# Kernel tuning notes

Measured on AMD Instinct MI355X. Metric: run time of the kernel, lower is better.

The kernel has to match this reference:

```python
import jax, jax.numpy as jnp
import numpy as np

M = 32          # option['m']
ETA = 1e-4      # option['eta']
THRES = 1e-12
NUM_DATA = 20000
NUM_FEAT = 1024


def setup_inputs() -> dict:
    key = jax.random.key(0)
    k1, k2 = jax.random.split(key)
    inputs_matrix = jax.random.normal(k1, (NUM_DATA, NUM_FEAT), dtype=jnp.float32)
    outputs = jax.random.normal(k2, (NUM_DATA,), dtype=jnp.float32)
    return {"inputs_matrix": inputs_matrix, "outputs": outputs}


def reference(inputs_matrix, outputs):
    """SFTRL_CCFM.online_learning (task='reg').

    Note on faithfulness: in the original torch code the negative-sketch
    branch (sign > 0) is guarded by `elif self.row_count_n == 2*m - 1`, and
    row_count_n starts at 0 and is only incremented inside that branch, so
    it is unreachable; BT_N stays identically zero and contributes 0 to
    `scalar`. We therefore only carry the positive sketch BT_P.
    """
    m, eta, thres = M, ETA, THRES
    two_m = 2 * m
    d = inputs_matrix.shape[1]

    def shrink(BT_P):
        # Frequent-Directions style shrink via SVD of the 2m x 2m Gram matrix.
        G = BT_P.T @ BT_P                                  # (2m, 2m)
        U, S, _ = jnp.linalg.svd(G)                        # S sorted descending
        S = jnp.where(S <= thres, 0.0, S)
        nnz = jnp.sum(S > 0).astype(jnp.int32)
        inv_sqrt = jnp.where(S > 0, 1.0 / jnp.sqrt(jnp.where(S > 0, S, 1.0)), 0.0)
        V = (BT_P @ U) * inv_sqrt[None, :]                 # (d, 2m); cols >= nnz are 0
        j = jnp.arange(two_m)
        # nnz >= m branch: keep m-1 cols scaled by sqrt(S_j - S_m), zero-pad rest.
        scale_big = jnp.where(j < m - 1, jnp.sqrt(jnp.maximum(S - S[m], 0.0)), 0.0)
        # nnz < m branch: keep nnz cols scaled by sqrt(S_j), zero-pad rest.
        scale_small = jnp.where(j < nnz, jnp.sqrt(S), 0.0)
        ge = nnz >= m
        scale = jnp.where(ge, scale_big, scale_small)
        return V * scale[None, :], jnp.where(ge, jnp.int32(m - 1), nnz)

    def step(carry, xs):
        BT_P, rc_p = carry
        alpha, bi = xs                                     # alpha: (d,)
        BPa = BT_P.T @ alpha                               # (2m,)
        scalar = BPa @ BPa                                 # BT_N == 0 -> its term vanishes
        sign = 2.0 * (scalar - bi)                         # grad of squared loss (task='reg')

        def do_update(args):
            B, rc = args
            rc = rc + 1                                    # original writes AFTER incrementing
            B = B.at[:, rc].set(jnp.sqrt(-eta * sign) * alpha)
            B, rc = jax.lax.cond(rc == two_m - 1, shrink, lambda Bp: (Bp, rc), B)
            return B, rc

        BT_P, rc_p = jax.lax.cond(sign <= 0.0, do_update, lambda a: a, (BT_P, rc_p))
        return (BT_P, rc_p), scalar

    init = (jnp.zeros((d, two_m), inputs_matrix.dtype), jnp.int32(0))
    _, preds = jax.lax.scan(step, init, (inputs_matrix, outputs))
    return preds
```

## Files before the change

### kernel.cpp

```cpp
#include <hip/hip_runtime.h>
#include <hip/hip_cooperative_groups.h>
#include <math.h>

namespace cg = cooperative_groups;

#define NDATA   20000
#define DFEAT   1024
#define TWO_M   64
#define MM      32
#define ETA_F   1e-4f
#define THRES_F 1e-12f
#define NSWEEP  8
#define NBLK    256
#define NTHR    1024
#define NW      (NBLK*(NTHR/64))
#define CH      384
#define BIGF    3.0e38f

#define O_CTL    0
#define O_CNT    256
#define O_ACCT   1280
#define O_ACCK   1536
#define O_TTIME  1792
#define O_BT     2048
#define O_BASE   264192
#define O_SCV    344192
#define O_FLAG   424192
#define O_CL0    504192
#define O_LA     584192
#define O_LB     664192
#define O_CHT    744192
#define O_CHB    746240
#define O_CHS    748288
#define O_D      750336

#define C_NACC 0
#define C_RC   1
#define C_SHR  2
#define C_TS   3
#define C_RCA  4
#define C_DONE 5

#define TG(r,c)     SH[(r)*257 + (c)]
#define SG(cb,idx)  SH[16448 + (cb)*4096 + (idx)]
#define SU(cb,idx)  SH[24640 + (cb)*4096 + (idx)]

__device__ __forceinline__ float wave_sum(float v) {
    v += __shfl_xor(v, 1);  v += __shfl_xor(v, 2);  v += __shfl_xor(v, 4);
    v += __shfl_xor(v, 8);  v += __shfl_xor(v, 16); v += __shfl_xor(v, 32);
    return v;
}
__device__ __forceinline__ int wave_min_i(int v) {
    v = min(v, __shfl_xor(v, 1));  v = min(v, __shfl_xor(v, 2));
    v = min(v, __shfl_xor(v, 4));  v = min(v, __shfl_xor(v, 8));
    v = min(v, __shfl_xor(v, 16)); v = min(v, __shfl_xor(v, 32));
    return v;
}
__device__ __forceinline__ void pair_from(int p, int &a, int &b) {
    int a_ = 0, rem = p;
    while (rem >= 64 - a_) { rem -= 64 - a_; ++a_; }
    a = a_; b = a_ + rem;
}
__device__ __forceinline__ float dot16(float4 x0, float4 x1, float4 x2, float4 x3,
                                       float4 y0, float4 y1, float4 y2, float4 y3) {
    float d = x0.x*y0.x + x0.y*y0.y + x0.z*y0.z + x0.w*y0.w;
    d += x1.x*y1.x + x1.y*y1.y + x1.z*y1.z + x1.w*y1.w;
    d += x2.x*y2.x + x2.y*y2.y + x2.z*y2.z + x2.w*y2.w;
    d += x3.x*y3.x + x3.y*y3.y + x3.z*y3.z + x3.w*y3.w;
    return d;
}
__device__ __forceinline__ int lbound(const int* arr, int n, int key) {
    int lo = 0, hi = n;
    while (lo < hi) { int mid = (lo + hi) >> 1; if (arr[mid] > key) hi = mid; else lo = mid + 1; }
    return lo;
}

__device__ void finalize_range(const float* __restrict__ A, const float* __restrict__ base,
                               const float* __restrict__ Bt, const int* __restrict__ ttime,
                               float* __restrict__ out,
                               int lo, int hi, int jlo, int jhi, int gw, int lane)
{
    for (int t = lo + gw; t <= hi; t += NW) {
        const float4* At = (const float4*)(A + (size_t)t * DFEAT);
        float4 a0 = At[lane*4+0], a1 = At[lane*4+1], a2 = At[lane*4+2], a3 = At[lane*4+3];
        float o = base[t];
        for (int jc = jlo; jc <= jhi; ++jc) {
            if (ttime[jc] >= t) break;
            const float4* Bj = (const float4*)(Bt + (size_t)jc * DFEAT);
            float d = dot16(a0, a1, a2, a3,
                            Bj[lane*4+0], Bj[lane*4+1], Bj[lane*4+2], Bj[lane*4+3]);
            d = wave_sum(d);
            o += d * d;
        }
        if (lane == 0) out[t] = o;
    }
}

__device__ void build_D(const float* __restrict__ A, const int* __restrict__ listP,
                        int clen, float* __restrict__ D, int w, int lane)
{
    if (w >= CH * 8) return;
    int i  = w >> 3;
    int of = w & 7;
    if (i >= clen) return;
    const float4* Ai = (const float4*)(A + (size_t)listP[i] * DFEAT);
    float4 a0 = Ai[lane*4+0], a1 = Ai[lane*4+1], a2 = Ai[lane*4+2], a3 = Ai[lane*4+3];
    for (int j = i + 1 + of; j < clen; j += 8) {
        const float4* Aj = (const float4*)(A + (size_t)listP[j] * DFEAT);
        float d = dot16(a0, a1, a2, a3,
                        Aj[lane*4+0], Aj[lane*4+1], Aj[lane*4+2], Aj[lane*4+3]);
        d = wave_sum(d);
        if (lane == 0) D[(size_t)i * CH + j] = d;
    }
}

__device__ void phase_prepare(const float* __restrict__ A, const float* __restrict__ Y,
                              float* __restrict__ scv, int* __restrict__ flag,
                              const int* __restrict__ listP, int lenL,
                              const int* __restrict__ accT, const float* __restrict__ accK, int nacc,
                              int* __restrict__ chT, float* __restrict__ chB, float* __restrict__ chS,
                              float* __restrict__ D, int* __restrict__ counts,
                              float* SH, int* s_cnt,
                              int bid, int tid, int wv, int lane, int gw)
{
    int clen = min(lenL, CH);
    for (int i = bid * NTHR + tid; i < clen; i += NBLK * NTHR) {
        int t = listP[i];
        chT[i] = t;
        chB[i] = Y[t];
    }
    const int hs = (CH + NBLK - 1) / NBLK;
    int h0 = min(bid * hs, clen), h1 = min(h0 + hs, clen);
    int tailLen = lenL > CH ? lenL - CH : 0;
    int ts2 = (tailLen + NBLK - 1) / NBLK;
    int t0 = CH + min(bid * ts2, tailLen), t1 = min(t0 + ts2, lenL);
    if (tid == 0) *s_cnt = 0;
    __syncthreads();

    for (int jb = 0; jb < nacc; jb += 16) {
        int nj = min(16, nacc - jb);
        if (wv < nj) {
            const float4* Ar = (const float4*)(A + (size_t)accT[jb + wv] * DFEAT);
            float4* S4 = (float4*)SH;
            for (int q = 0; q < 4; ++q) S4[wv * 256 + lane * 4 + q] = Ar[lane * 4 + q];
        }
        __syncthreads();
        const float4* S4 = (const float4*)SH;
        for (int pass = 0; pass < 2; ++pass) {
            int lo = pass ? t0 : h0, hi = pass ? t1 : h1;
            for (int e = lo + wv; e < hi; e += 16) {
                int t = listP[e];
                const float4* At = (const float4*)(A + (size_t)t * DFEAT);
                float4 a0 = At[lane*4+0], a1 = At[lane*4+1], a2 = At[lane*4+2], a3 = At[lane*4+3];
                float cacc = 0.f;
                for (int j = 0; j < nj; ++j) {
                    float d = dot16(a0, a1, a2, a3,
                                    S4[j*256+lane*4+0], S4[j*256+lane*4+1],
                                    S4[j*256+lane*4+2], S4[j*256+lane*4+3]);
                    d = wave_sum(d);
                    float v = accK[jb + j] * d;
                    cacc += v * v;
                }
                if (lane == 0) scv[t] += cacc;
            }
        }
        __syncthreads();
    }

    for (int e = h0 + tid; e < h1; e += NTHR) {
        int t = listP[e];
        float sc = scv[t];
        int alive = (sc <= Y[t]) ? 1 : 0;
        flag[t] = alive;
        chS[e] = alive ? sc : BIGF;
    }
    for (int e = t0 + tid; e < t1; e += NTHR) {
        int t = listP[e];
        float sc = scv[t];
        int alive = (sc <= Y[t]) ? 1 : 0;
        flag[t] = alive;
        if (alive) atomicAdd(s_cnt, 1);
    }
    __syncthreads();
    if (tid == 0) counts[bid] = *s_cnt;

    build_D(A, listP, clen, D, gw, lane);
}

__device__ int scatter_and_total(const int* __restrict__ listCur, int lenCur,
                                 const int* __restrict__ flag, const int* __restrict__ counts,
                                 int* __restrict__ listNxt, int bid, int tid, int wv, int lane)
{
    int tailLen = lenCur > CH ? lenCur - CH : 0;
    int ts2 = (tailLen + NBLK - 1) / NBLK;
    int e0 = min(bid * ts2, tailLen), e1 = min(e0 + ts2, tailLen);
    if (wv == 0 && e1 > e0) {
        int dst = 0;
        for (int b = 0; b < bid; ++b) dst += counts[b];
        for (int w0 = e0; w0 < e1; w0 += 64) {
            int idx = w0 + lane;
            int tt = 0, fl = 0;
            if (idx < e1) { tt = listCur[CH + idx]; fl = flag[tt]; }
            unsigned long long mb = __ballot(fl);
            int pos = (int)__popcll(mb & ((1ull << lane) - 1ull));
            if (fl) listNxt[dst + pos] = tt;
            dst += (int)__popcll(mb);
        }
    }
    int tot = 0;
    for (int b = 0; b < NBLK; ++b) tot += counts[b];
    return tot;
}

__device__ void resolve_blk0(const float* __restrict__ A, float* __restrict__ Bt,
                             int* __restrict__ ttime,
                             const int* __restrict__ chT, const float* __restrict__ chB,
                             const float* __restrict__ chS, const float* __restrict__ D,
                             int* __restrict__ ctl, int* __restrict__ accT, float* __restrict__ accK,
                             int chunkLen, int tailTotal,
                             float* accL, float* bbL, int* s_red, int* s_imin,
                             int* accTl, float* accKl, int tid, int wv, int lane)
{
    int rc0 = ctl[C_RC];
    if (tid < CH) {
        accL[tid] = (tid < chunkLen) ? chS[tid] : BIGF;
        bbL[tid]  = (tid < chunkLen) ? chB[tid] : -BIGF;
    }
    __syncthreads();
    int rcl = rc0, naccL = 0, shr = 0, tsv = NDATA;
    for (;;) {
        int cand = 0x7FFFFFFF;
        if (tid < chunkLen && accL[tid] <= bbL[tid]) cand = tid;
        cand = wave_min_i(cand);
        if (lane == 0) s_red[wv] = cand;
        __syncthreads();
        if (wv == 0) {
            int v = (lane < 16) ? s_red[lane] : 0x7FFFFFFF;
            v = wave_min_i(v);
            if (lane == 0) *s_imin = v;
        }
        __syncthreads();
        int im = *s_imin;
        if (im == 0x7FFFFFFF) break;
        float sc = accL[im], b = bbL[im];
        float kap = sqrtf(2.f * ETA_F * (b - sc));
        __syncthreads();
        rcl += 1;
        if (tid == 0) { accTl[naccL] = chT[im]; accKl[naccL] = kap; }
        naccL += 1;
        if (tid > im && tid < chunkLen) {
            float dv = D[(size_t)im * CH + tid];
            float v = kap * dv;
            accL[tid] += v * v;
        }
        if (tid <= im && tid < CH) accL[tid] = BIGF;
        if (rcl == TWO_M - 1) { shr = 1; tsv = chT[im]; }
        __syncthreads();
        if (shr) break;
    }
    __syncthreads();
    for (int q = 0; q < naccL; ++q) {
        int colr = rc0 + 1 + q;
        int tq = accTl[q];
        float kq = accKl[q];
        Bt[(size_t)colr * DFEAT + tid] = kq * A[(size_t)tq * DFEAT + tid];
        if (tid == 0) ttime[colr] = tq;
    }
    if (tid < naccL) { accT[tid] = accTl[tid]; accK[tid] = accKl[tid]; }
    if (tid == 0) {
        ctl[C_NACC] = naccL;
        ctl[C_RC]   = rcl;
        ctl[C_SHR]  = shr;
        ctl[C_TS]   = tsv;
        ctl[C_DONE] = (!shr && naccL == 0 && tailTotal == 0) ? 1 : 0;
    }
}

__device__ void jacobi_shrink(float* __restrict__ Bt, int* __restrict__ ctl, float* SH,
                              float* s_rotA, float* s_rotB, int* s_prt,
                              float* s_S, float* s_Ss, int* s_perm, int* s_misc, int tid)
{
    float acc0 = 0.f, acc1 = 0.f, acc2 = 0.f;
    int a0i, b0i, a1i, b1i, a2i, b2i;
    pair_from(tid, a0i, b0i);
    pair_from(tid + 1024, a1i, b1i);
    pair_from((tid < 32) ? (tid + 2048) : 0, a2i, b2i);
    for (int c = 0; c < 4; ++c) {
        __syncthreads();
        for (int q = tid; q < 64 * 64; q += NTHR) {
            int jj = q >> 6, d4 = q & 63;
            float4 v = ((const float4*)(Bt + (size_t)jj * DFEAT + c * 256))[d4];
            TG(jj, d4*4+0) = v.x; TG(jj, d4*4+1) = v.y;
            TG(jj, d4*4+2) = v.z; TG(jj, d4*4+3) = v.w;
        }
        __syncthreads();
        for (int dd = 0; dd < 256; ++dd) {
            acc0 += TG(a0i, dd) * TG(b0i, dd);
            acc1 += TG(a1i, dd) * TG(b1i, dd);
            acc2 += TG(a2i, dd) * TG(b2i, dd);
        }
    }
    SG(0, a0i*64+b0i) = acc0; SG(0, b0i*64+a0i) = acc0;
    SG(0, a1i*64+b1i) = acc1; SG(0, b1i*64+a1i) = acc1;
    if (tid < 32) { SG(0, a2i*64+b2i) = acc2; SG(0, b2i*64+a2i) = acc2; }
    for (int e4 = 0; e4 < 4; ++e4) {
        int e = tid + e4 * 1024;
        SU(0, e) = ((e >> 6) == (e & 63)) ? 1.f : 0.f;
    }
    __syncthreads();

    int cur = 0;
    for (int sw = 0; sw < NSWEEP; ++sw) {
        for (int r = 0; r < 63; ++r) {
            if (tid < 32) {
                int p_, q_;
                if (tid == 0) { p_ = 63; q_ = r; }
                else { p_ = (r + tid) % 63; q_ = (r + 63 - tid) % 63; }
                float gpp = SG(cur, p_*64+p_);
                float gqq = SG(cur, q_*64+q_);
                float gpq = SG(cur, p_*64+q_);
                float cc = 1.f, sn = 0.f;
                if (fabsf(gpq) > 1e-20f) {
                    float tau = (gqq - gpp) / (2.f * gpq);
                    float tt  = (tau >= 0.f ? 1.f : -1.f) / (fabsf(tau) + sqrtf(1.f + tau * tau));
                    cc = 1.f / sqrtf(1.f + tt * tt);
                    sn = tt * cc;
                }
                s_rotA[p_] = cc; s_rotB[p_] = -sn; s_prt[p_] = q_;
                s_rotA[q_] = cc; s_rotB[q_] = sn;  s_prt[q_] = p_;
            }
            __syncthreads();
            float ng[4], nu[4];
            for (int e4 = 0; e4 < 4; ++e4) {
                int e = tid + e4 * 1024;
                int row = e >> 6, col = e & 63;
                int pr = s_prt[row], pc = s_prt[col];
                float ar = s_rotA[row], br = s_rotB[row];
                float ac = s_rotA[col], bc = s_rotB[col];
                ng[e4] = ar*ac*SG(cur, row*64+col) + br*ac*SG(cur, pr*64+col)
                       + ar*bc*SG(cur, row*64+pc)  + br*bc*SG(cur, pr*64+pc);
                nu[e4] = ac*SU(cur, row*64+col) + bc*SU(cur, row*64+pc);
            }
            for (int e4 = 0; e4 < 4; ++e4) {
                int e = tid + e4 * 1024;
                SG(cur ^ 1, e) = ng[e4];
                SU(cur ^ 1, e) = nu[e4];
            }
            __syncthreads();
            cur ^= 1;
        }
    }

    if (tid < 64) {
        float lam = SG(cur, tid*64+tid);
        if (lam <= THRES_F) lam = 0.f;
        s_S[tid] = lam;
    }
    __syncthreads();
    if (tid < 64) {
        float my = s_S[tid];
        int rank = 0;
        for (int i = 0; i < 64; ++i) {
            float o = s_S[i];
            rank += ((o > my) || (o == my && i < tid)) ? 1 : 0;
        }
        s_perm[rank] = tid;
        s_Ss[rank]   = my;
    }
    __syncthreads();
    if (tid == 0) {
        int nz = 0;
        for (int i = 0; i < 64; ++i) nz += (s_Ss[i] > 0.f) ? 1 : 0;
        s_misc[0] = nz;
        s_misc[1] = (nz >= MM) ? 1 : 0;
    }
    __syncthreads();
    const int nnz = s_misc[0];
    const int ge  = s_misc[1];
    const float S32 = s_Ss[MM];

    for (int e4 = 0; e4 < 4; ++e4) {
        int e = tid + e4 * 1024;
        int kk = e >> 6, jn = e & 63;
        float Sj = s_Ss[jn];
        float f;
        if (ge) f = (jn < MM - 1 && Sj > 0.f) ? sqrtf(fmaxf(Sj - S32, 0.f) / Sj) : 0.f;
        else    f = (jn < nnz) ? 1.f : 0.f;
        SG(0, kk*64+jn) = SU(cur, kk*64 + s_perm[jn]) * f;
    }
    __syncthreads();

    for (int c = 0; c < 4; ++c) {
        __syncthreads();
        for (int q = tid; q < 64 * 64; q += NTHR) {
            int jj = q >> 6, d4 = q & 63;
            float4 v = ((const float4*)(Bt + (size_t)jj * DFEAT + c * 256))[d4];
            TG(jj, d4*4+0) = v.x; TG(jj, d4*4+1) = v.y;
            TG(jj, d4*4+2) = v.z; TG(jj, d4*4+3) = v.w;
        }
        __syncthreads();
        for (int q = tid; q < 64 * 256; q += NTHR) {
            int dd = q & 255, jn = q >> 8;
            float sum = 0.f;
            for (int kk = 0; kk < 64; ++kk)
                sum += TG(kk, dd) * SG(0, kk*64+jn);
            Bt[(size_t)jn * DFEAT + c * 256 + dd] = sum;
        }
    }
    __syncthreads();
    if (tid == 0) {
        int rcn = ge ? (MM - 1) : nnz;
        ctl[C_RCA] = rcn;
        ctl[C_RC]  = rcn;
    }
}

__device__ void recompute_rows(const float* __restrict__ A, const float* __restrict__ Y,
                               const float* __restrict__ Bt,
                               float* __restrict__ scv, float* __restrict__ base,
                               int* __restrict__ flag, int ts,
                               float* SH, int tid, int wv, int lane, int gw)
{
    int nrows = NDATA - 1 - ts;
    int npair = (nrows + 1) >> 1;
    for (int h = 0; h < 2; ++h) {
        {
            const float4* B4 = (const float4*)Bt;
            float4* S4 = (float4*)SH;
            for (int q = 0; q < 4; ++q) {
                S4[wv * 256 + lane*4 + q]        = B4[(size_t)(h*32 + wv) * 256 + lane*4 + q];
                S4[(wv+16) * 256 + lane*4 + q]   = B4[(size_t)(h*32 + wv + 16) * 256 + lane*4 + q];
            }
        }
        __syncthreads();
        const float4* S4 = (const float4*)SH;
        for (int p = gw; p < npair; p += NW) {
            int tA = ts + 1 + 2*p;
            int tB = tA + 1;
            bool hasB = tB < NDATA;
            const float4* Aa = (const float4*)(A + (size_t)tA * DFEAT);
            float4 x0 = Aa[lane*4+0], x1 = Aa[lane*4+1], x2 = Aa[lane*4+2], x3 = Aa[lane*4+3];
            float4 y0 = make_float4(0,0,0,0), y1 = y0, y2 = y0, y3 = y0;
            if (hasB) {
                const float4* Ab = (const float4*)(A + (size_t)tB * DFEAT);
                y0 = Ab[lane*4+0]; y1 = Ab[lane*4+1]; y2 = Ab[lane*4+2]; y3 = Ab[lane*4+3];
            }
            float s1 = 0.f, s2 = 0.f;
            for (int j = 0; j < 32; ++j) {
                float4 b0 = S4[j*256+lane*4+0], b1 = S4[j*256+lane*4+1],
                       b2 = S4[j*256+lane*4+2], b3 = S4[j*256+lane*4+3];
                float d1 = dot16(x0,x1,x2,x3,b0,b1,b2,b3);
                d1 = wave_sum(d1);
                s1 += d1 * d1;
                float d2 = dot16(y0,y1,y2,y3,b0,b1,b2,b3);
                d2 = wave_sum(d2);
                s2 += d2 * d2;
            }
            if (lane == 0) {
                if (h == 0) {
                    scv[tA] = s1;
                    if (hasB) scv[tB] = s2;
                } else {
                    float f1 = scv[tA] + s1;
                    scv[tA] = f1; base[tA] = f1; flag[tA] = (f1 <= Y[tA]) ? 1 : 0;
                    if (hasB) {
                        float f2 = scv[tB] + s2;
                        scv[tB] = f2; base[tB] = f2; flag[tB] = (f2 <= Y[tB]) ? 1 : 0;
                    }
                }
            }
        }
        __syncthreads();
    }
}

__global__ __launch_bounds__(NTHR, 4)
void sftrl_v3(const float* __restrict__ A, const float* __restrict__ Y,
              float* __restrict__ out, char* __restrict__ ws)
{
    cg::grid_group grid = cg::this_grid();
    const int tid = threadIdx.x, lane = tid & 63, wv = tid >> 6, bid = blockIdx.x;
    const int gw = bid * 16 + wv;

    int*   ctl    = (int*)(ws + O_CTL);
    int*   counts = (int*)(ws + O_CNT);
    int*   accT   = (int*)(ws + O_ACCT);
    float* accK   = (float*)(ws + O_ACCK);
    int*   ttime  = (int*)(ws + O_TTIME);
    float* Bt     = (float*)(ws + O_BT);
    float* base   = (float*)(ws + O_BASE);
    float* scv    = (float*)(ws + O_SCV);
    int*   flag   = (int*)(ws + O_FLAG);
    int*   cl0    = (int*)(ws + O_CL0);
    int*   LA     = (int*)(ws + O_LA);
    int*   LB     = (int*)(ws + O_LB);
    int*   chT    = (int*)(ws + O_CHT);
    float* chB    = (float*)(ws + O_CHB);
    float* chS    = (float*)(ws + O_CHS);
    float* D      = (float*)(ws + O_D);

    __shared__ float SH[32832];
    __shared__ float s_rotA[64], s_rotB[64];
    __shared__ int   s_prt[64];
    __shared__ float s_S[64], s_Ss[64];
    __shared__ int   s_perm[64], s_misc[2];
    __shared__ float accL[CH], bbL[CH];
    __shared__ int   s_red[16];
    __shared__ int   s_imin, s_cnt;
    __shared__ int   accTl[64];
    __shared__ float accKl[64];

    const int rb = (NDATA + NBLK - 1) / NBLK;
    int r0 = min(bid * rb, NDATA), r1 = min(r0 + rb, NDATA);
    if (tid == 0) s_cnt = 0;
    __syncthreads();
    for (int t = r0 + tid; t < r1; t += NTHR) {
        base[t] = 0.f; scv[t] = 0.f;
        int f = (0.f <= Y[t]) ? 1 : 0;
        flag[t] = f;
        if (f) atomicAdd(&s_cnt, 1);
    }
    for (int i = bid * NTHR + tid; i < TWO_M * DFEAT; i += NBLK * NTHR) Bt[i] = 0.f;
    if (bid == 0 && tid < 16) ctl[tid] = 0;
    __syncthreads();
    if (tid == 0) counts[bid] = s_cnt;
    __threadfence();
    grid.sync();

    {
        int dst = 0;
        for (int b = 0; b < bid; ++b) dst += counts[b];
        if (wv == 0) {
            for (int w0 = r0; w0 < r1; w0 += 64) {
                int t = w0 + lane;
                int fl = (t < r1) ? flag[t] : 0;
                unsigned long long mb = __ballot(fl);
                int pos = (int)__popcll(mb & ((1ull << lane) - 1ull));
                if (fl) cl0[dst + pos] = t;
                dst += (int)__popcll(mb);
            }
        }
    }
    int ncand = 0;
    for (int b = 0; b < NBLK; ++b) ncand += counts[b];
    __threadfence();
    grid.sync();

    int* listCur = cl0;
    int  lenCur  = ncand;
    phase_prepare(A, Y, scv, flag, listCur, lenCur, accT, accK, 0,
                  chT, chB, chS, D, counts, SH, &s_cnt, bid, tid, wv, lane, gw);
    __threadfence();
    grid.sync();

    int fin_hi = -1, seg_lo = 1;

    for (;;) {
        int chunkLen = min(lenCur, CH);
        int* listNxt = (listCur == LA) ? LB : LA;

        int tailTotal = scatter_and_total(listCur, lenCur, flag, counts, listNxt,
                                          bid, tid, wv, lane);
        if (bid == 0)
            resolve_blk0(A, Bt, ttime, chT, chB, chS, D, ctl, accT, accK,
                         chunkLen, tailTotal, accL, bbL, s_red, &s_imin,
                         accTl, accKl, tid, wv, lane);
        __threadfence();
        grid.sync();

        int nacc = ctl[C_NACC], rc = ctl[C_RC], shr = ctl[C_SHR], done = ctl[C_DONE];
        if (done) {
            finalize_range(A, base, Bt, ttime, out, fin_hi + 1, NDATA - 1, seg_lo, rc, gw, lane);
            return;
        }
        if (shr) {
            int ts = ctl[C_TS];
            finalize_range(A, base, Bt, ttime, out, fin_hi + 1, ts, seg_lo, rc - 1, gw, lane);
            __threadfence();
            grid.sync();
            int cstart = lbound(cl0, ncand, ts);
            int clen2 = min(ncand - cstart, CH);
            if (bid == 0) {
                jacobi_shrink(Bt, ctl, SH, s_rotA, s_rotB, s_prt, s_S, s_Ss, s_perm, s_misc, tid);
            } else {
                if (bid == 1) {
                    for (int i = tid; i < clen2; i += NTHR) {
                        int t = cl0[cstart + i];
                        chT[i] = t; chB[i] = Y[t];
                    }
                }
                build_D(A, cl0 + cstart, clen2, D, (bid - 1) * 16 + wv, lane);
            }
            __threadfence();
            grid.sync();
            int rcn = ctl[C_RCA];
            seg_lo = rcn + 1; fin_hi = ts;
            recompute_rows(A, Y, Bt, scv, base, flag, ts, SH, tid, wv, lane, gw);
            __threadfence();
            grid.sync();
            listCur = cl0 + cstart; lenCur = ncand - cstart;
            for (int i = bid * NTHR + tid; i < clen2; i += NBLK * NTHR) {
                int t = chT[i];
                chS[i] = flag[t] ? scv[t] : BIGF;
            }
            {
                int tailLen = lenCur > CH ? lenCur - CH : 0;
                int ts2 = (tailLen + NBLK - 1) / NBLK;
                int e0 = min(bid * ts2, tailLen), e1 = min(e0 + ts2, tailLen);
                if (tid == 0) s_cnt = 0;
                __syncthreads();
                for (int e = e0 + tid; e < e1; e += NTHR) {
                    int t = listCur[CH + e];
                    if (flag[t]) atomicAdd(&s_cnt, 1);
                }
                __syncthreads();
                if (tid == 0) counts[bid] = s_cnt;
            }
            __threadfence();
            grid.sync();
            continue;
        }
        int lenNxt = tailTotal;
        phase_prepare(A, Y, scv, flag, listNxt, lenNxt, accT, accK, nacc,
                      chT, chB, chS, D, counts, SH, &s_cnt, bid, tid, wv, lane, gw);
        __threadfence();
        grid.sync();
        listCur = listNxt; lenCur = lenNxt;
    }
}

extern "C" void kernel_launch(void* const* d_in, const int* in_sizes, int n_in,
                              void* d_out, int out_size, void* d_ws, size_t ws_size,
                              hipStream_t stream) {
    (void)in_sizes; (void)n_in; (void)ws_size; (void)out_size;
    const float* A = (const float*)d_in[0];
    const float* Y = (const float*)d_in[1];
    float* out = (float*)d_out;
    char* ws = (char*)d_ws;
    void* kargs[] = { (void*)&A, (void*)&Y, (void*)&out, (void*)&ws };
    hipLaunchCooperativeKernel((void*)sftrl_v3, dim3(NBLK), dim3(NTHR), kargs, 0, stream);
}
```

Baseline: 1.507 ms.

## Replace grid.sync with custom barrier, enlarge candidate chunk, coalesce row loads

Replaces cooperative-groups grid.sync with a hand-rolled atomic generation barrier, and replaces the serial per-block prefix sums over counts with a wave-level scan. Row slice loads change from lane*4+q to lane+64*q for coalesced access, and build_D is regridded to four waves per row. The chunk size becomes a template parameter, 1024 when the workspace is large enough, so more candidates are resolved per round. Risks: the custom barrier depends on zeroed workspace and correct memory ordering, and the larger chunk raises pairwise Gram work per round.

New measurement: 4.075 ms (median of 4 runs). 170% more time.

```diff
diff --git a/kernel.cpp b/kernel.cpp
--- a/kernel.cpp
+++ b/kernel.cpp
@@ -1,8 +1,5 @@
 #include <hip/hip_runtime.h>
-#include <hip/hip_cooperative_groups.h>
 #include <math.h>
-
-namespace cg = cooperative_groups;
 
 #define NDATA   20000
 #define DFEAT   1024
@@ -14,7 +11,6 @@
 #define NBLK    256
 #define NTHR    1024
 #define NW      (NBLK*(NTHR/64))
-#define CH      384
 #define BIGF    3.0e38f
 
 #define O_CTL    0
@@ -30,9 +26,9 @@
 #define O_LA     584192
 #define O_LB     664192
 #define O_CHT    744192
-#define O_CHB    746240
-#define O_CHS    748288
-#define O_D      750336
+#define O_CHB    748288
+#define O_CHS    752384
+#define O_D      756480
 
 #define C_NACC 0
 #define C_RC   1
@@ -44,6 +40,8 @@
 #define TG(r,c)     SH[(r)*257 + (c)]
 #define SG(cb,idx)  SH[16448 + (cb)*4096 + (idx)]
 #define SU(cb,idx)  SH[24640 + (cb)*4096 + (idx)]
+
+#define LD_SLICE(P,v0,v1,v2,v3) do { v0=(P)[lane]; v1=(P)[lane+64]; v2=(P)[lane+128]; v3=(P)[lane+192]; } while(0)
 
 __device__ __forceinline__ float wave_sum(float v) {
     v += __shfl_xor(v, 1);  v += __shfl_xor(v, 2);  v += __shfl_xor(v, 4);
@@ -75,6 +73,43 @@
     return lo;
 }
 
+__device__ __forceinline__ void gbar(int* __restrict__ bar, int* __restrict__ gen) {
+    __threadfence();
+    __syncthreads();
+    if (threadIdx.x == 0) {
+        int g = __hip_atomic_load(gen, __ATOMIC_RELAXED, __HIP_MEMORY_SCOPE_AGENT);
+        int a = __hip_atomic_fetch_add(bar, 1, __ATOMIC_ACQ_REL, __HIP_MEMORY_SCOPE_AGENT);
+        if (a == NBLK - 1) {
+            __hip_atomic_store(bar, 0, __ATOMIC_RELAXED, __HIP_MEMORY_SCOPE_AGENT);
+            __hip_atomic_store(gen, g + 1, __ATOMIC_RELEASE, __HIP_MEMORY_SCOPE_AGENT);
+        } else {
+            while (__hip_atomic_load(gen, __ATOMIC_ACQUIRE, __HIP_MEMORY_SCOPE_AGENT) == g)
+                __builtin_amdgcn_s_sleep(1);
+        }
+    }
+    __syncthreads();
+    __builtin_amdgcn_fence(__ATOMIC_ACQUIRE, "agent");
+}
+
+__device__ __forceinline__ void counts_scan(const int* __restrict__ counts, int bid, int lane,
+                                            int* prefix_out, int* total_out) {
+    const int4 c4 = ((const int4*)counts)[lane];
+    int s = c4.x + c4.y + c4.z + c4.w;
+    int inc = s;
+    for (int off = 1; off < 64; off <<= 1) {
+        int o = __shfl_up(inc, off);
+        if (lane >= off) inc += o;
+    }
+    int total = __shfl(inc, 63);
+    int lanepre = inc - s;
+    int L = bid >> 2, r = bid & 3;
+    int grouppre = __shfl(lanepre, L);
+    int4 cg = ((const int4*)counts)[L];
+    int part = (r > 0 ? cg.x : 0) + (r > 1 ? cg.y : 0) + (r > 2 ? cg.z : 0);
+    *prefix_out = grouppre + part;
+    *total_out  = total;
+}
+
 __device__ void finalize_range(const float* __restrict__ A, const float* __restrict__ base,
                                const float* __restrict__ Bt, const int* __restrict__ ttime,
                                float* __restrict__ out,
@@ -82,13 +117,13 @@
 {
     for (int t = lo + gw; t <= hi; t += NW) {
         const float4* At = (const float4*)(A + (size_t)t * DFEAT);
-        float4 a0 = At[lane*4+0], a1 = At[lane*4+1], a2 = At[lane*4+2], a3 = At[lane*4+3];
+        float4 a0, a1, a2, a3; LD_SLICE(At, a0, a1, a2, a3);
         float o = base[t];
         for (int jc = jlo; jc <= jhi; ++jc) {
             if (ttime[jc] >= t) break;
             const float4* Bj = (const float4*)(Bt + (size_t)jc * DFEAT);
-            float d = dot16(a0, a1, a2, a3,
-                            Bj[lane*4+0], Bj[lane*4+1], Bj[lane*4+2], Bj[lane*4+3]);
+            float4 b0, b1, b2, b3; LD_SLICE(Bj, b0, b1, b2, b3);
+            float d = dot16(a0, a1, a2, a3, b0, b1, b2, b3);
             d = wave_sum(d);
             o += d * d;
         }
@@ -96,24 +131,26 @@
     }
 }
 
+template<int CHV>
 __device__ void build_D(const float* __restrict__ A, const int* __restrict__ listP,
-                        int clen, float* __restrict__ D, int w, int lane)
-{
-    if (w >= CH * 8) return;
-    int i  = w >> 3;
-    int of = w & 7;
-    if (i >= clen) return;
-    const float4* Ai = (const float4*)(A + (size_t)listP[i] * DFEAT);
-    float4 a0 = Ai[lane*4+0], a1 = Ai[lane*4+1], a2 = Ai[lane*4+2], a3 = Ai[lane*4+3];
-    for (int j = i + 1 + of; j < clen; j += 8) {
-        const float4* Aj = (const float4*)(A + (size_t)listP[j] * DFEAT);
-        float d = dot16(a0, a1, a2, a3,
-                        Aj[lane*4+0], Aj[lane*4+1], Aj[lane*4+2], Aj[lane*4+3]);
-        d = wave_sum(d);
-        if (lane == 0) D[(size_t)i * CH + j] = d;
-    }
-}
-
+                        int clen, float* __restrict__ D, int wave_id, int n_waves, int lane)
+{
+    const int WPR = 4;
+    for (int ii = wave_id; ii < clen * WPR; ii += n_waves) {
+        int i = ii >> 2, of = ii & 3;
+        const float4* Ai = (const float4*)(A + (size_t)listP[i] * DFEAT);
+        float4 a0, a1, a2, a3; LD_SLICE(Ai, a0, a1, a2, a3);
+        for (int j = i + 1 + of; j < clen; j += WPR) {
+            const float4* Aj = (const float4*)(A + (size_t)listP[j] * DFEAT);
+            float4 b0, b1, b2, b3; LD_SLICE(Aj, b0, b1, b2, b3);
+            float d = dot16(a0, a1, a2, a3, b0, b1, b2, b3);
+            d = wave_sum(d);
+            if (lane == 0) D[(size_t)i * CHV + j] = d;
+        }
+    }
+}
+
+template<int CHV>
 __device__ void phase_prepare(const float* __restrict__ A, const float* __restrict__ Y,
                               float* __restrict__ scv, int* __restrict__ flag,
                               const int* __restrict__ listP, int lenL,
@@ -123,17 +160,17 @@
                               float* SH, int* s_cnt,
                               int bid, int tid, int wv, int lane, int gw)
 {
-    int clen = min(lenL, CH);
+    int clen = min(lenL, CHV);
     for (int i = bid * NTHR + tid; i < clen; i += NBLK * NTHR) {
         int t = listP[i];
         chT[i] = t;
         chB[i] = Y[t];
     }
-    const int hs = (CH + NBLK - 1) / NBLK;
+    const int hs = (CHV + NBLK - 1) / NBLK;
     int h0 = min(bid * hs, clen), h1 = min(h0 + hs, clen);
-    int tailLen = lenL > CH ? lenL - CH : 0;
+    int tailLen = lenL > CHV ? lenL - CHV : 0;
     int ts2 = (tailLen + NBLK - 1) / NBLK;
-    int t0 = CH + min(bid * ts2, tailLen), t1 = min(t0 + ts2, lenL);
+    int t0 = CHV + min(bid * ts2, tailLen), t1 = min(t0 + ts2, lenL);
     if (tid == 0) *s_cnt = 0;
     __syncthreads();
 
@@ -142,7 +179,7 @@
         if (wv < nj) {
             const float4* Ar = (const float4*)(A + (size_t)accT[jb + wv] * DFEAT);
             float4* S4 = (float4*)SH;
-            for (int q = 0; q < 4; ++q) S4[wv * 256 + lane * 4 + q] = Ar[lane * 4 + q];
+            for (int q = 0; q < 4; ++q) S4[wv * 256 + lane + 64 * q] = Ar[lane + 64 * q];
         }
         __syncthreads();
         const float4* S4 = (const float4*)SH;
@@ -151,12 +188,12 @@
             for (int e = lo + wv; e < hi; e += 16) {
                 int t = listP[e];
                 const float4* At = (const float4*)(A + (size_t)t * DFEAT);
-                float4 a0 = At[lane*4+0], a1 = At[lane*4+1], a2 = At[lane*4+2], a3 = At[lane*4+3];
+                float4 a0, a1, a2, a3; LD_SLICE(At, a0, a1, a2, a3);
                 float cacc = 0.f;
                 for (int j = 0; j < nj; ++j) {
                     float d = dot16(a0, a1, a2, a3,
-                                    S4[j*256+lane*4+0], S4[j*256+lane*4+1],
-                                    S4[j*256+lane*4+2], S4[j*256+lane*4+3]);
+                                    S4[j*256+lane], S4[j*256+lane+64],
+                                    S4[j*256+lane+128], S4[j*256+lane+192]);
                     d = wave_sum(d);
                     float v = accK[jb + j] * d;
                     cacc += v * v;
@@ -184,34 +221,35 @@
     __syncthreads();
     if (tid == 0) counts[bid] = *s_cnt;
 
-    build_D(A, listP, clen, D, gw, lane);
-}
-
+    build_D<CHV>(A, listP, clen, D, gw, NW, lane);
+}
+
+template<int CHV>
 __device__ int scatter_and_total(const int* __restrict__ listCur, int lenCur,
                                  const int* __restrict__ flag, const int* __restrict__ counts,
                                  int* __restrict__ listNxt, int bid, int tid, int wv, int lane)
 {
-    int tailLen = lenCur > CH ? lenCur - CH : 0;
+    int tailLen = lenCur > CHV ? lenCur - CHV : 0;
     int ts2 = (tailLen + NBLK - 1) / NBLK;
     int e0 = min(bid * ts2, tailLen), e1 = min(e0 + ts2, tailLen);
+    int pre, tot;
+    counts_scan(counts, bid, lane, &pre, &tot);
     if (wv == 0 && e1 > e0) {
-        int dst = 0;
-        for (int b = 0; b < bid; ++b) dst += counts[b];
+        int dst = pre;
         for (int w0 = e0; w0 < e1; w0 += 64) {
             int idx = w0 + lane;
             int tt = 0, fl = 0;
-            if (idx < e1) { tt = listCur[CH + idx]; fl = flag[tt]; }
+            if (idx < e1) { tt = listCur[CHV + idx]; fl = flag[tt]; }
             unsigned long long mb = __ballot(fl);
             int pos = (int)__popcll(mb & ((1ull << lane) - 1ull));
             if (fl) listNxt[dst + pos] = tt;
             dst += (int)__popcll(mb);
         }
     }
-    int tot = 0;
-    for (int b = 0; b < NBLK; ++b) tot += counts[b];
     return tot;
 }
 
+template<int CHV>
 __device__ void resolve_blk0(const float* __restrict__ A, float* __restrict__ Bt,
                              int* __restrict__ ttime,
                              const int* __restrict__ chT, const float* __restrict__ chB,
@@ -222,7 +260,7 @@
                              int* accTl, float* accKl, int tid, int wv, int lane)
 {
     int rc0 = ctl[C_RC];
-    if (tid < CH) {
+    if (tid < CHV) {
         accL[tid] = (tid < chunkLen) ? chS[tid] : BIGF;
         bbL[tid]  = (tid < chunkLen) ? chB[tid] : -BIGF;
     }
@@ -249,11 +287,11 @@
         if (tid == 0) { accTl[naccL] = chT[im]; accKl[naccL] = kap; }
         naccL += 1;
         if (tid > im && tid < chunkLen) {
-            float dv = D[(size_t)im * CH + tid];
+            float dv = D[(size_t)im * CHV + tid];
             float v = kap * dv;
             accL[tid] += v * v;
         }
-        if (tid <= im && tid < CH) accL[tid] = BIGF;
+        if (tid <= im && tid < CHV) accL[tid] = BIGF;
         if (rcl == TWO_M - 1) { shr = 1; tsv = chT[im]; }
         __syncthreads();
         if (shr) break;
@@ -428,8 +466,8 @@
             const float4* B4 = (const float4*)Bt;
             float4* S4 = (float4*)SH;
             for (int q = 0; q < 4; ++q) {
-                S4[wv * 256 + lane*4 + q]        = B4[(size_t)(h*32 + wv) * 256 + lane*4 + q];
-                S4[(wv+16) * 256 + lane*4 + q]   = B4[(size_t)(h*32 + wv + 16) * 256 + lane*4 + q];
+                S4[wv * 256 + lane + 64*q]      = B4[(size_t)(h*32 + wv) * 256 + lane + 64*q];
+                S4[(wv+16) * 256 + lane + 64*q] = B4[(size_t)(h*32 + wv + 16) * 256 + lane + 64*q];
             }
         }
         __syncthreads();
@@ -439,16 +477,16 @@
             int tB = tA + 1;
             bool hasB = tB < NDATA;
             const float4* Aa = (const float4*)(A + (size_t)tA * DFEAT);
-            float4 x0 = Aa[lane*4+0], x1 = Aa[lane*4+1], x2 = Aa[lane*4+2], x3 = Aa[lane*4+3];
+            float4 x0, x1, x2, x3; LD_SLICE(Aa, x0, x1, x2, x3);
             float4 y0 = make_float4(0,0,0,0), y1 = y0, y2 = y0, y3 = y0;
             if (hasB) {
                 const float4* Ab = (const float4*)(A + (size_t)tB * DFEAT);
-                y0 = Ab[lane*4+0]; y1 = Ab[lane*4+1]; y2 = Ab[lane*4+2]; y3 = Ab[lane*4+3];
+                LD_SLICE(Ab, y0, y1, y2, y3);
             }
             float s1 = 0.f, s2 = 0.f;
             for (int j = 0; j < 32; ++j) {
-                float4 b0 = S4[j*256+lane*4+0], b1 = S4[j*256+lane*4+1],
-                       b2 = S4[j*256+lane*4+2], b3 = S4[j*256+lane*4+3];
+                float4 b0 = S4[j*256+lane],     b1 = S4[j*256+lane+64],
+                       b2 = S4[j*256+lane+128], b3 = S4[j*256+lane+192];
                 float d1 = dot16(x0,x1,x2,x3,b0,b1,b2,b3);
                 d1 = wave_sum(d1);
                 s1 += d1 * d1;
@@ -474,15 +512,17 @@
     }
 }
 
+template<int CHV>
 __global__ __launch_bounds__(NTHR, 4)
-void sftrl_v3(const float* __restrict__ A, const float* __restrict__ Y,
+void sftrl_v4(const float* __restrict__ A, const float* __restrict__ Y,
               float* __restrict__ out, char* __restrict__ ws)
 {
-    cg::grid_group grid = cg::this_grid();
     const int tid = threadIdx.x, lane = tid & 63, wv = tid >> 6, bid = blockIdx.x;
     const int gw = bid * 16 + wv;
 
     int*   ctl    = (int*)(ws + O_CTL);
+    int*   bar    = (int*)(ws + 128);
+    int*   gen    = (int*)(ws + 192);
     int*   counts = (int*)(ws + O_CNT);
     int*   accT   = (int*)(ws + O_ACCT);
     float* accK   = (float*)(ws + O_ACCK);
@@ -499,12 +539,12 @@
     float* chS    = (float*)(ws + O_CHS);
     float* D      = (float*)(ws + O_D);
 
-    __shared__ float SH[32832];
+    __shared__ __attribute__((aligned(16))) float SH[32832];
     __shared__ float s_rotA[64], s_rotB[64];
     __shared__ int   s_prt[64];
     __shared__ float s_S[64], s_Ss[64];
     __shared__ int   s_perm[64], s_misc[2];
-    __shared__ float accL[CH], bbL[CH];
+    __shared__ float accL[CHV], bbL[CHV];
     __shared__ int   s_red[16];
     __shared__ int   s_imin, s_cnt;
     __shared__ int   accTl[64];
@@ -524,13 +564,15 @@
     if (bid == 0 && tid < 16) ctl[tid] = 0;
     __syncthreads();
     if (tid == 0) counts[bid] = s_cnt;
-    __threadfence();
-    grid.sync();
-
+    gbar(bar, gen);
+
+    int ncand;
     {
-        int dst = 0;
-        for (int b = 0; b < bid; ++b) dst += counts[b];
+        int pre, tot;
+        counts_scan(counts, bid, lane, &pre, &tot);
+        ncand = tot;
         if (wv == 0) {
+            int dst = pre;
             for (int w0 = r0; w0 < r1; w0 += 64) {
                 int t = w0 + lane;
                 int fl = (t < r1) ? flag[t] : 0;
@@ -541,32 +583,27 @@
             }
         }
     }
-    int ncand = 0;
-    for (int b = 0; b < NBLK; ++b) ncand += counts[b];
-    __threadfence();
-    grid.sync();
+    gbar(bar, gen);
 
     int* listCur = cl0;
     int  lenCur  = ncand;
-    phase_prepare(A, Y, scv, flag, listCur, lenCur, accT, accK, 0,
-                  chT, chB, chS, D, counts, SH, &s_cnt, bid, tid, wv, lane, gw);
-    __threadfence();
-    grid.sync();
+    phase_prepare<CHV>(A, Y, scv, flag, listCur, lenCur, accT, accK, 0,
+                       chT, chB, chS, D, counts, SH, &s_cnt, bid, tid, wv, lane, gw);
+    gbar(bar, gen);
 
     int fin_hi = -1, seg_lo = 1;
 
     for (;;) {
-        int chunkLen = min(lenCur, CH);
+        int chunkLen = min(lenCur, CHV);
         int* listNxt = (listCur == LA) ? LB : LA;
 
-        int tailTotal = scatter_and_total(listCur, lenCur, flag, counts, listNxt,
-                                          bid, tid, wv, lane);
+        int tailTotal = scatter_and_total<CHV>(listCur, lenCur, flag, counts, listNxt,
+                                               bid, tid, wv, lane);
         if (bid == 0)
-            resolve_blk0(A, Bt, ttime, chT, chB, chS, D, ctl, accT, accK,
-                         chunkLen, tailTotal, accL, bbL, s_red, &s_imin,
-                         accTl, accKl, tid, wv, lane);
-        __threadfence();
-        grid.sync();
+            resolve_blk0<CHV>(A, Bt, ttime, chT, chB, chS, D, ctl, accT, accK,
+                              chunkLen, tailTotal, accL, bbL, s_red, &s_imin,
+                              accTl, accKl, tid, wv, lane);
+        gbar(bar, gen);
 
         int nacc = ctl[C_NACC], rc = ctl[C_RC], shr = ctl[C_SHR], done = ctl[C_DONE];
         if (done) {
@@ -576,10 +613,9 @@
         if (shr) {
             int ts = ctl[C_TS];
             finalize_range(A, base, Bt, ttime, out, fin_hi + 1, ts, seg_lo, rc - 1, gw, lane);
-            __threadfence();
-            grid.sync();
+            gbar(bar, gen);
             int cstart = lbound(cl0, ncand, ts);
-            int clen2 = min(ncand - cstart, CH);
+            int clen2 = min(ncand - cstart, CHV);
             if (bid == 0) {
                 jacobi_shrink(Bt, ctl, SH, s_rotA, s_rotB, s_prt, s_S, s_Ss, s_perm, s_misc, tid);
             } else {
@@ -589,42 +625,38 @@
                         chT[i] = t; chB[i] = Y[t];
                     }
                 }
-                build_D(A, cl0 + cstart, clen2, D, (bid - 1) * 16 + wv, lane);
-            }
-            __threadfence();
-            grid.sync();
+                build_D<CHV>(A, cl0 + cstart, clen2, D, (bid - 1) * 16 + wv, 255 * 16, lane);
+            }
+            gbar(bar, gen);
             int rcn = ctl[C_RCA];
             seg_lo = rcn + 1; fin_hi = ts;
             recompute_rows(A, Y, Bt, scv, base, flag, ts, SH, tid, wv, lane, gw);
-            __threadfence();
-            grid.sync();
+            gbar(bar, gen);
             listCur = cl0 + cstart; lenCur = ncand - cstart;
             for (int i = bid * NTHR + tid; i < clen2; i += NBLK * NTHR) {
                 int t = chT[i];
                 chS[i] = flag[t] ? scv[t] : BIGF;
             }
             {
-                int tailLen = lenCur > CH ? lenCur - CH : 0;
+                int tailLen = lenCur > CHV ? lenCur - CHV : 0;
                 int ts2 = (tailLen + NBLK - 1) / NBLK;
                 int e0 = min(bid * ts2, tailLen), e1 = min(e0 + ts2, tailLen);
                 if (tid == 0) s_cnt = 0;
                 __syncthreads();
                 for (int e = e0 + tid; e < e1; e += NTHR) {
-                    int t = listCur[CH + e];
+                    int t = listCur[CHV + e];
                     if (flag[t]) atomicAdd(&s_cnt, 1);
                 }
                 __syncthreads();
                 if (tid == 0) counts[bid] = s_cnt;
             }
-            __threadfence();
-            grid.sync();
+            gbar(bar, gen);
             continue;
         }
         int lenNxt = tailTotal;
-        phase_prepare(A, Y, scv, flag, listNxt, lenNxt, accT, accK, nacc,
-                      chT, chB, chS, D, counts, SH, &s_cnt, bid, tid, wv, lane, gw);
-        __threadfence();
-        grid.sync();
+        phase_prepare<CHV>(A, Y, scv, flag, listNxt, lenNxt, accT, accK, nacc,
+                           chT, chB, chS, D, counts, SH, &s_cnt, bid, tid, wv, lane, gw);
+        gbar(bar, gen);
         listCur = listNxt; lenCur = lenNxt;
     }
 }
@@ -632,11 +664,21 @@
 extern "C" void kernel_launch(void* const* d_in, const int* in_sizes, int n_in,
                               void* d_out, int out_size, void* d_ws, size_t ws_size,
                               hipStream_t stream) {
-    (void)in_sizes; (void)n_in; (void)ws_size; (void)out_size;
+    (void)in_sizes; (void)n_in; (void)out_size;
     const float* A = (const float*)d_in[0];
     const float* Y = (const float*)d_in[1];
     float* out = (float*)d_out;
     char* ws = (char*)d_ws;
+
+    hipMemsetAsync(ws, 0, 256, stream);
+
     void* kargs[] = { (void*)&A, (void*)&Y, (void*)&out, (void*)&ws };
-    hipLaunchCooperativeKernel((void*)sftrl_v3, dim3(NBLK), dim3(NTHR), kargs, 0, stream);
-}
+    size_t need1024 = (size_t)O_D + (size_t)4 * 1024 * 1024;
+    if (ws_size >= need1024) {
+        hipLaunchCooperativeKernel((void*)sftrl_v4<1024>, dim3(NBLK), dim3(NTHR),
+                                   kargs, 0, stream);
+    } else {
+        hipLaunchCooperativeKernel((void*)sftrl_v4<384>, dim3(NBLK), dim3(NTHR),
+                                   kargs, 0, stream);
+    }
+}
```
